# Optimization experiments

Hardware: AMD Instinct MI355X
Metric: run time of the kernel (lower is better)

The kernel has to match this reference:

```python
import jax, jax.numpy as jnp
import numpy as np

D_MODEL = 1024
N_HEADS = 16
HEAD_DIM = D_MODEL // N_HEADS
SOFTMAX_SCALE = 1.0 / np.sqrt(HEAD_DIM).astype(np.float32)


def setup_inputs() -> dict:
    key = jax.random.key(0)
    k1, k2, k3, k4, k5 = jax.random.split(key, 5)
    B, S = 2, 2048
    bound_qkv = 1.0 / np.sqrt(D_MODEL)
    x = jax.random.normal(k1, (B, S, D_MODEL), dtype=jnp.float32)
    # torch nn.Linear stores weight as [out_features, in_features]
    Wqkv_w = jax.random.uniform(k2, (3 * D_MODEL, D_MODEL), jnp.float32, -bound_qkv, bound_qkv)
    Wqkv_b = jax.random.uniform(k3, (3 * D_MODEL,), jnp.float32, -bound_qkv, bound_qkv)
    Wout_w = jax.random.uniform(k4, (D_MODEL, D_MODEL), jnp.float32, -bound_qkv, bound_qkv)
    Wout_b = jax.random.uniform(k5, (D_MODEL,), jnp.float32, -bound_qkv, bound_qkv)
    return {"x": x, "Wqkv_w": Wqkv_w, "Wqkv_b": Wqkv_b, "Wout_w": Wout_w, "Wout_b": Wout_b}


def reference(x, Wqkv_w, Wqkv_b, Wout_w, Wout_b):
    B, S, D = x.shape
    # fused QKV projection
    qkv = jnp.einsum('bsd,ed->bse', x, Wqkv_w) + Wqkv_b  # [B, S, 3D]
    q, k, v = jnp.split(qkv, 3, axis=2)
    # b s (h d) -> b h s d
    q = q.reshape(B, S, N_HEADS, HEAD_DIM).transpose(0, 2, 1, 3)
    k = k.reshape(B, S, N_HEADS, HEAD_DIM).transpose(0, 2, 1, 3)
    v = v.reshape(B, S, N_HEADS, HEAD_DIM).transpose(0, 2, 1, 3)
    attn = jnp.einsum('bhsd,bhtd->bhst', q, k) * SOFTMAX_SCALE
    attn = jax.nn.softmax(attn, axis=-1)
    ctx = jnp.einsum('bhst,bhtd->bhsd', attn, v)
    ctx = ctx.transpose(0, 2, 1, 3).reshape(B, S, D)
    out = jnp.einsum('bsd,ed->bse', ctx, Wout_w) + Wout_b
    return out
```

## Files before the change

kernel.cpp:

```cpp
#include <hip/hip_runtime.h>
#include <hip/hip_bf16.h>

typedef __attribute__((ext_vector_type(8))) __bf16 bfrag;
typedef __attribute__((ext_vector_type(4))) float f32x4;
typedef __attribute__((ext_vector_type(16))) float f32x16;
typedef __attribute__((ext_vector_type(8))) unsigned short u16x8;
typedef __attribute__((ext_vector_type(4))) unsigned short u16x4;
typedef __attribute__((ext_vector_type(4))) unsigned int u32x4;

#define SEQ 2048
#define NH 16
#define HD 64
#define DMODEL 1024
#define MTOT 4096
#define QSCALE 0.18033688011112042f

static __device__ __forceinline__ unsigned short f2bf(float f) {
  unsigned int u = __builtin_bit_cast(unsigned int, f);
  u += 0x7FFFu + ((u >> 16) & 1u);
  return (unsigned short)(u >> 16);
}

static __device__ __forceinline__ unsigned cvt_pk_bf16(float lo, float hi) {
  unsigned r;
  asm("v_cvt_pk_bf16_f32 %0, %1, %2" : "=v"(r) : "v"(lo), "v"(hi));
  return r;
}

static __device__ __forceinline__ float rmax16(const f32x16 v) {
  float a0 = fmaxf(v[0], v[1]), a1 = fmaxf(v[2], v[3]);
  float a2 = fmaxf(v[4], v[5]), a3 = fmaxf(v[6], v[7]);
  float a4 = fmaxf(v[8], v[9]), a5 = fmaxf(v[10], v[11]);
  float a6 = fmaxf(v[12], v[13]), a7 = fmaxf(v[14], v[15]);
  float b0 = fmaxf(a0, a1), b1 = fmaxf(a2, a3), b2 = fmaxf(a4, a5), b3 = fmaxf(a6, a7);
  return fmaxf(fmaxf(b0, b1), fmaxf(b2, b3));
}

static __device__ __forceinline__ float rsum16(const f32x16 v) {
  float a0 = v[0] + v[1], a1 = v[2] + v[3], a2 = v[4] + v[5], a3 = v[6] + v[7];
  float a4 = v[8] + v[9], a5 = v[10] + v[11], a6 = v[12] + v[13], a7 = v[14] + v[15];
  float b0 = a0 + a1, b1 = a2 + a3, b2 = a4 + a5, b3 = a6 + a7;
  return (b0 + b1) + (b2 + b3);
}

__global__ __launch_bounds__(256) void cvt_bf16_kernel(const float* __restrict__ in,
                                                       unsigned short* __restrict__ out,
                                                       int n8) {
  int i = blockIdx.x * 256 + threadIdx.x;
  if (i >= n8) return;
  const float4* p = reinterpret_cast<const float4*>(in) + (size_t)i * 2;
  float4 a = p[0], b = p[1];
  u16x8 o;
  o[0] = f2bf(a.x); o[1] = f2bf(a.y); o[2] = f2bf(a.z); o[3] = f2bf(a.w);
  o[4] = f2bf(b.x); o[5] = f2bf(b.y); o[6] = f2bf(b.z); o[7] = f2bf(b.w);
  *(reinterpret_cast<u16x8*>(out) + i) = o;
}

#define GLDS(gp, lp)                                                       \
  __builtin_amdgcn_global_load_lds(                                        \
      (const __attribute__((address_space(1))) void*)(gp),                 \
      (__attribute__((address_space(3))) void*)(lp), 16, 0, 0)

template <int EPI>
__global__ __launch_bounds__(256) void gemm_bt_kernel(
    const unsigned short* __restrict__ A, const unsigned short* __restrict__ B,
    const float* __restrict__ bias, unsigned short* __restrict__ q_out,
    unsigned short* __restrict__ k_out, unsigned short* __restrict__ v_out,
    float* __restrict__ f_out, int M, int N, int K) {
  __shared__ __align__(16) unsigned short As[128 * 32];
  __shared__ __align__(16) unsigned short Bs[128 * 32];
  const int t = threadIdx.x;
  const int l = t & 63, w = t >> 6;
  const int m0 = blockIdx.y * 128, n0 = blockIdx.x * 128;
  const int wrow = (w >> 1) * 64, wcol = (w & 1) * 64;
  const int lrow = l & 15, lk = (l >> 4) * 8;
  const int srow = t >> 2;
  const int scol = ((t & 3) ^ (srow & 3)) * 8;
  f32x4 acc[4][4] = {};
  for (int k0 = 0; k0 < K; k0 += 32) {
    __syncthreads();
    GLDS(A + (size_t)(m0 + srow) * K + k0 + scol, As + (size_t)t * 8);
    GLDS(A + (size_t)(m0 + srow + 64) * K + k0 + scol, As + 2048 + (size_t)t * 8);
    GLDS(B + (size_t)(n0 + srow) * K + k0 + scol, Bs + (size_t)t * 8);
    GLDS(B + (size_t)(n0 + srow + 64) * K + k0 + scol, Bs + 2048 + (size_t)t * 8);
    __syncthreads();
    bfrag af[4], bf[4];
#pragma unroll
    for (int mt = 0; mt < 4; ++mt) {
      int row = wrow + mt * 16 + lrow;
      af[mt] = *(const bfrag*)&As[row * 32 + (lk ^ ((row & 3) << 3))];
    }
#pragma unroll
    for (int nt = 0; nt < 4; ++nt) {
      int row = wcol + nt * 16 + lrow;
      bf[nt] = *(const bfrag*)&Bs[row * 32 + (lk ^ ((row & 3) << 3))];
    }
#pragma unroll
    for (int mt = 0; mt < 4; ++mt)
#pragma unroll
      for (int nt = 0; nt < 4; ++nt)
        acc[mt][nt] =
            __builtin_amdgcn_mfma_f32_16x16x32_bf16(af[mt], bf[nt], acc[mt][nt], 0, 0, 0);
  }
#pragma unroll
  for (int nt = 0; nt < 4; ++nt) {
    int gn = n0 + wcol + nt * 16 + lrow;
    float bv = bias[gn];
    if constexpr (EPI == 0) {
      int sel = gn >> 10;
      int e = gn & 1023;
      int h = e >> 6, d = e & 63;
#pragma unroll
      for (int mt = 0; mt < 4; ++mt) {
#pragma unroll
        for (int r = 0; r < 4; ++r) {
          int gm = m0 + wrow + mt * 16 + (l >> 4) * 4 + r;
          int b = gm >> 11, s = gm & 2047;
          float fv = acc[mt][nt][r] + bv;
          if (sel == 0)
            q_out[((size_t)(b * NH + h) * SEQ + s) * HD + d] = f2bf(fv * QSCALE);
          else if (sel == 1)
            k_out[((size_t)(b * NH + h) * SEQ + s) * HD + d] = f2bf(fv);
          else
            v_out[((size_t)(b * NH + h) * HD + d) * SEQ + s] = f2bf(fv);
        }
      }
    } else {
#pragma unroll
      for (int mt = 0; mt < 4; ++mt) {
#pragma unroll
        for (int r = 0; r < 4; ++r) {
          int gm = m0 + wrow + mt * 16 + (l >> 4) * 4 + r;
          f_out[(size_t)gm * N + gn] = acc[mt][nt][r] + bv;
        }
      }
    }
  }
}

__global__ __launch_bounds__(256, 2)
void attn_kernel(const unsigned short* __restrict__ Q,
                 const unsigned short* __restrict__ Km,
                 const unsigned short* __restrict__ Vt,
                 unsigned short* __restrict__ Ctx) {
  __shared__ __align__(16) unsigned short Ks[2][4096];
  __shared__ __align__(16) unsigned short Vs[2][4096];
  const int t = threadIdx.x;
  const int l = t & 63, w = t >> 6;
  const int q31 = l & 31, h = l >> 5;
  const int lid = blockIdx.y * gridDim.x + blockIdx.x;
  const int bh = (lid & 7) * 4 + ((lid >> 3) >> 4);
  const int q0 = ((lid >> 3) & 15) * 128 + w * 32;
  const unsigned short* qb = Q + (size_t)bh * SEQ * HD;
  const unsigned short* kb = Km + (size_t)bh * SEQ * HD;
  const unsigned short* vb = Vt + (size_t)bh * HD * SEQ;

  bfrag qf[4];
#pragma unroll
  for (int c = 0; c < 4; ++c)
    qf[c] = *(const bfrag*)&qb[(size_t)(q0 + q31) * HD + c * 16 + h * 8];

  f32x16 acc0 = {}, acc1 = {};
  float m = -3e38f, lsum = 0.f;

  const int srow = t >> 3;
  const int ssw = ((t & 7) ^ (srow & 7)) * 8;

  GLDS(kb + (size_t)srow * HD + ssw, &Ks[0][0] + t * 8);
  GLDS(kb + (size_t)(32 + srow) * HD + ssw, &Ks[0][0] + 2048 + t * 8);
  GLDS(vb + (size_t)srow * SEQ + ssw, &Vs[0][0] + t * 8);
  GLDS(vb + (size_t)(32 + srow) * SEQ + ssw, &Vs[0][0] + 2048 + t * 8);
  __syncthreads();

  const int swz = q31 & 7;

#pragma unroll 1
  for (int t2 = 0; t2 < 32; ++t2) {
    const unsigned short* Kc = &Ks[t2 & 1][0];
    const unsigned short* Vc = &Vs[t2 & 1][0];
    if (t2 < 31) {
      unsigned short* kd = &Ks[(t2 + 1) & 1][0];
      unsigned short* vd = &Vs[(t2 + 1) & 1][0];
      const int kvn = (t2 + 1) * 64;
      GLDS(kb + (size_t)(kvn + srow) * HD + ssw, kd + t * 8);
      GLDS(kb + (size_t)(kvn + 32 + srow) * HD + ssw, kd + 2048 + t * 8);
      GLDS(vb + (size_t)srow * SEQ + kvn + ssw, vd + t * 8);
      GLDS(vb + (size_t)(32 + srow) * SEQ + kvn + ssw, vd + 2048 + t * 8);
    }
    bfrag kf[8], vf[8];
#pragma unroll
    for (int i = 0; i < 8; ++i) {
      const int off = ((i >> 2) * 32 + q31) * 64 + ((((i & 3) * 2 + h) ^ swz) * 8);
      kf[i] = *(const bfrag*)&Kc[off];
      vf[i] = *(const bfrag*)&Vc[off];
    }
    f32x16 s0 = {}, s1 = {};
#pragma unroll
    for (int c = 0; c < 4; ++c) {
      s0 = __builtin_amdgcn_mfma_f32_32x32x16_bf16(kf[c], qf[c], s0, 0, 0, 0);
      s1 = __builtin_amdgcn_mfma_f32_32x32x16_bf16(kf[4 + c], qf[c], s1, 0, 0, 0);
    }
    float tm = fmaxf(rmax16(s0), rmax16(s1));
    tm = fmaxf(tm, __shfl_xor(tm, 32));
    if (!__all(tm - m <= 8.f)) {
      float mn = fmaxf(m, tm);
      float al = __builtin_amdgcn_exp2f(m - mn);
      m = mn;
      lsum *= al;
#pragma unroll
      for (int r = 0; r < 16; ++r) {
        acc0[r] *= al;
        acc1[r] *= al;
      }
    }
#pragma unroll
    for (int r = 0; r < 16; ++r) s0[r] = __builtin_amdgcn_exp2f(s0[r] - m);
#pragma unroll
    for (int r = 0; r < 16; ++r) s1[r] = __builtin_amdgcn_exp2f(s1[r] - m);
    float ps = rsum16(s0) + rsum16(s1);
    ps += __shfl_xor(ps, 32);
    lsum += ps;
#pragma unroll
    for (int cg = 0; cg < 4; ++cg) {
      const f32x16 sv = (cg < 2) ? s0 : s1;
      const int bse = (cg & 1) * 8;
      unsigned pk0 = cvt_pk_bf16(sv[bse + 0], sv[bse + 1]);
      unsigned pk1 = cvt_pk_bf16(sv[bse + 2], sv[bse + 3]);
      unsigned pk2 = cvt_pk_bf16(sv[bse + 4], sv[bse + 5]);
      unsigned pk3 = cvt_pk_bf16(sv[bse + 6], sv[bse + 7]);
      auto w02 = __builtin_amdgcn_permlane32_swap(pk0, pk2, false, false);
      auto w13 = __builtin_amdgcn_permlane32_swap(pk1, pk3, false, false);
      u32x4 bw = {(unsigned)w02[0], (unsigned)w13[0], (unsigned)w02[1], (unsigned)w13[1]};
      bfrag pb = __builtin_bit_cast(bfrag, bw);
      acc0 = __builtin_amdgcn_mfma_f32_32x32x16_bf16(vf[cg], pb, acc0, 0, 0, 0);
      acc1 = __builtin_amdgcn_mfma_f32_32x32x16_bf16(vf[4 + cg], pb, acc1, 0, 0, 0);
    }
    __syncthreads();
  }

  const int b = bh >> 4, head = bh & 15;
  const float inv = __builtin_amdgcn_rcpf(lsum);
  unsigned short* cp = Ctx + ((size_t)(b * SEQ + (q0 + q31)) * NH + head) * HD;
#pragma unroll
  for (int dt = 0; dt < 2; ++dt) {
    const f32x16 av = dt ? acc1 : acc0;
#pragma unroll
    for (int rq = 0; rq < 4; ++rq) {
      u16x4 o;
#pragma unroll
      for (int rr = 0; rr < 4; ++rr) o[rr] = f2bf(av[rq * 4 + rr] * inv);
      *(u16x4*)&cp[dt * 32 + rq * 8 + h * 4] = o;
    }
  }
}

extern "C" void kernel_launch(void* const* d_in, const int* in_sizes, int n_in,
                              void* d_out, int out_size, void* d_ws, size_t ws_size,
                              hipStream_t stream) {
  const float* x = (const float*)d_in[0];
  const float* wqkv = (const float*)d_in[1];
  const float* bqkv = (const float*)d_in[2];
  const float* wout = (const float*)d_in[3];
  const float* bout = (const float*)d_in[4];
  float* out = (float*)d_out;

  unsigned short* xb = (unsigned short*)d_ws;
  unsigned short* wqkvb = xb + (size_t)MTOT * DMODEL;
  unsigned short* woutb = wqkvb + (size_t)3 * DMODEL * DMODEL;
  unsigned short* qb = woutb + (size_t)DMODEL * DMODEL;
  unsigned short* kb = qb + (size_t)32 * SEQ * HD;
  unsigned short* vtb = kb + (size_t)32 * SEQ * HD;
  unsigned short* ctxb = vtb + (size_t)32 * SEQ * HD;

  {
    int n8 = MTOT * DMODEL / 8;
    cvt_bf16_kernel<<<(n8 + 255) / 256, 256, 0, stream>>>(x, xb, n8);
  }
  {
    int n8 = 3 * DMODEL * DMODEL / 8;
    cvt_bf16_kernel<<<(n8 + 255) / 256, 256, 0, stream>>>(wqkv, wqkvb, n8);
  }
  {
    int n8 = DMODEL * DMODEL / 8;
    cvt_bf16_kernel<<<(n8 + 255) / 256, 256, 0, stream>>>(wout, woutb, n8);
  }
  gemm_bt_kernel<0><<<dim3(3 * DMODEL / 128, MTOT / 128), 256, 0, stream>>>(
      xb, wqkvb, bqkv, qb, kb, vtb, nullptr, MTOT, 3 * DMODEL, DMODEL);
  attn_kernel<<<dim3(SEQ / 128, 32), 256, 0, stream>>>(qb, kb, vtb, ctxb);
  gemm_bt_kernel<1><<<dim3(DMODEL / 128, MTOT / 128), 256, 0, stream>>>(
      ctxb, woutb, bout, nullptr, nullptr, nullptr, out, MTOT, DMODEL, DMODEL);
}
```

Baseline: 137.7 us.

## Triple-buffer LDS staging in GEMM and attention with vmcnt-based waits

```diff
diff --git a/kernel.cpp b/kernel.cpp
--- a/kernel.cpp
+++ b/kernel.cpp
@@ -67,8 +67,8 @@
     const float* __restrict__ bias, unsigned short* __restrict__ q_out,
     unsigned short* __restrict__ k_out, unsigned short* __restrict__ v_out,
     float* __restrict__ f_out, int M, int N, int K) {
-  __shared__ __align__(16) unsigned short As[128 * 32];
-  __shared__ __align__(16) unsigned short Bs[128 * 32];
+  __shared__ __align__(16) unsigned short As[3][4096];
+  __shared__ __align__(16) unsigned short Bs[3][4096];
   const int t = threadIdx.x;
   const int l = t & 63, w = t >> 6;
   const int m0 = blockIdx.y * 128, n0 = blockIdx.x * 128;
@@ -77,23 +77,41 @@
   const int srow = t >> 2;
   const int scol = ((t & 3) ^ (srow & 3)) * 8;
   f32x4 acc[4][4] = {};
-  for (int k0 = 0; k0 < K; k0 += 32) {
-    __syncthreads();
-    GLDS(A + (size_t)(m0 + srow) * K + k0 + scol, As + (size_t)t * 8);
-    GLDS(A + (size_t)(m0 + srow + 64) * K + k0 + scol, As + 2048 + (size_t)t * 8);
-    GLDS(B + (size_t)(n0 + srow) * K + k0 + scol, Bs + (size_t)t * 8);
-    GLDS(B + (size_t)(n0 + srow + 64) * K + k0 + scol, Bs + 2048 + (size_t)t * 8);
-    __syncthreads();
+
+#define GSTAGE(buf, K0)                                                     \
+  do {                                                                      \
+    GLDS(A + (size_t)(m0 + srow) * K + (K0) + scol, &As[buf][0] + t * 8);   \
+    GLDS(A + (size_t)(m0 + srow + 64) * K + (K0) + scol,                    \
+         &As[buf][0] + 2048 + t * 8);                                       \
+    GLDS(B + (size_t)(n0 + srow) * K + (K0) + scol, &Bs[buf][0] + t * 8);   \
+    GLDS(B + (size_t)(n0 + srow + 64) * K + (K0) + scol,                    \
+         &Bs[buf][0] + 2048 + t * 8);                                       \
+  } while (0)
+
+  const int nsteps = K >> 5;
+  GSTAGE(0, 0);
+  GSTAGE(1, 32);
+#pragma unroll 1
+  for (int ks = 0; ks < nsteps; ++ks) {
+    if (ks < nsteps - 1)
+      asm volatile("s_waitcnt vmcnt(4)" ::: "memory");
+    else
+      asm volatile("s_waitcnt vmcnt(0)" ::: "memory");
+    __builtin_amdgcn_s_barrier();
+    __builtin_amdgcn_sched_barrier(0);
+    if (ks + 2 < nsteps) GSTAGE((ks + 2) % 3, (ks + 2) * 32);
+    const unsigned short* Ac = &As[ks % 3][0];
+    const unsigned short* Bc = &Bs[ks % 3][0];
     bfrag af[4], bf[4];
 #pragma unroll
     for (int mt = 0; mt < 4; ++mt) {
       int row = wrow + mt * 16 + lrow;
-      af[mt] = *(const bfrag*)&As[row * 32 + (lk ^ ((row & 3) << 3))];
+      af[mt] = *(const bfrag*)&Ac[row * 32 + (lk ^ ((row & 3) << 3))];
     }
 #pragma unroll
     for (int nt = 0; nt < 4; ++nt) {
       int row = wcol + nt * 16 + lrow;
-      bf[nt] = *(const bfrag*)&Bs[row * 32 + (lk ^ ((row & 3) << 3))];
+      bf[nt] = *(const bfrag*)&Bc[row * 32 + (lk ^ ((row & 3) << 3))];
     }
 #pragma unroll
     for (int mt = 0; mt < 4; ++mt)
@@ -102,6 +120,7 @@
         acc[mt][nt] =
             __builtin_amdgcn_mfma_f32_16x16x32_bf16(af[mt], bf[nt], acc[mt][nt], 0, 0, 0);
   }
+#undef GSTAGE
 #pragma unroll
   for (int nt = 0; nt < 4; ++nt) {
     int gn = n0 + wcol + nt * 16 + lrow;
@@ -143,8 +162,8 @@
                  const unsigned short* __restrict__ Km,
                  const unsigned short* __restrict__ Vt,
                  unsigned short* __restrict__ Ctx) {
-  __shared__ __align__(16) unsigned short Ks[2][4096];
-  __shared__ __align__(16) unsigned short Vs[2][4096];
+  __shared__ __align__(16) unsigned short Ks[3][4096];
+  __shared__ __align__(16) unsigned short Vs[3][4096];
   const int t = threadIdx.x;
   const int l = t & 63, w = t >> 6;
   const int q31 = l & 31, h = l >> 5;
@@ -166,27 +185,33 @@
   const int srow = t >> 3;
   const int ssw = ((t & 7) ^ (srow & 7)) * 8;
 
-  GLDS(kb + (size_t)srow * HD + ssw, &Ks[0][0] + t * 8);
-  GLDS(kb + (size_t)(32 + srow) * HD + ssw, &Ks[0][0] + 2048 + t * 8);
-  GLDS(vb + (size_t)srow * SEQ + ssw, &Vs[0][0] + t * 8);
-  GLDS(vb + (size_t)(32 + srow) * SEQ + ssw, &Vs[0][0] + 2048 + t * 8);
-  __syncthreads();
+#define STAGE(buf, T)                                                        \
+  do {                                                                       \
+    const int kv0_ = (T) * 64;                                               \
+    GLDS(kb + (size_t)(kv0_ + srow) * HD + ssw, &Ks[buf][0] + t * 8);        \
+    GLDS(kb + (size_t)(kv0_ + 32 + srow) * HD + ssw,                         \
+         &Ks[buf][0] + 2048 + t * 8);                                        \
+    GLDS(vb + (size_t)srow * SEQ + kv0_ + ssw, &Vs[buf][0] + t * 8);         \
+    GLDS(vb + (size_t)(32 + srow) * SEQ + kv0_ + ssw,                        \
+         &Vs[buf][0] + 2048 + t * 8);                                        \
+  } while (0)
+
+  STAGE(0, 0);
+  STAGE(1, 1);
 
   const int swz = q31 & 7;
 
 #pragma unroll 1
   for (int t2 = 0; t2 < 32; ++t2) {
-    const unsigned short* Kc = &Ks[t2 & 1][0];
-    const unsigned short* Vc = &Vs[t2 & 1][0];
-    if (t2 < 31) {
-      unsigned short* kd = &Ks[(t2 + 1) & 1][0];
-      unsigned short* vd = &Vs[(t2 + 1) & 1][0];
-      const int kvn = (t2 + 1) * 64;
-      GLDS(kb + (size_t)(kvn + srow) * HD + ssw, kd + t * 8);
-      GLDS(kb + (size_t)(kvn + 32 + srow) * HD + ssw, kd + 2048 + t * 8);
-      GLDS(vb + (size_t)srow * SEQ + kvn + ssw, vd + t * 8);
-      GLDS(vb + (size_t)(32 + srow) * SEQ + kvn + ssw, vd + 2048 + t * 8);
-    }
+    if (t2 < 31)
+      asm volatile("s_waitcnt vmcnt(4)" ::: "memory");
+    else
+      asm volatile("s_waitcnt vmcnt(0)" ::: "memory");
+    __builtin_amdgcn_s_barrier();
+    __builtin_amdgcn_sched_barrier(0);
+    if (t2 < 30) STAGE((t2 + 2) % 3, t2 + 2);
+    const unsigned short* Kc = &Ks[t2 % 3][0];
+    const unsigned short* Vc = &Vs[t2 % 3][0];
     bfrag kf[8], vf[8];
 #pragma unroll
     for (int i = 0; i < 8; ++i) {
@@ -195,11 +220,13 @@
       vf[i] = *(const bfrag*)&Vc[off];
     }
     f32x16 s0 = {}, s1 = {};
+    __builtin_amdgcn_s_setprio(1);
 #pragma unroll
     for (int c = 0; c < 4; ++c) {
       s0 = __builtin_amdgcn_mfma_f32_32x32x16_bf16(kf[c], qf[c], s0, 0, 0, 0);
       s1 = __builtin_amdgcn_mfma_f32_32x32x16_bf16(kf[4 + c], qf[c], s1, 0, 0, 0);
     }
+    __builtin_amdgcn_s_setprio(0);
     float tm = fmaxf(rmax16(s0), rmax16(s1));
     tm = fmaxf(tm, __shfl_xor(tm, 32));
     if (!__all(tm - m <= 8.f)) {
@@ -220,6 +247,7 @@
     float ps = rsum16(s0) + rsum16(s1);
     ps += __shfl_xor(ps, 32);
     lsum += ps;
+    __builtin_amdgcn_s_setprio(1);
 #pragma unroll
     for (int cg = 0; cg < 4; ++cg) {
       const f32x16 sv = (cg < 2) ? s0 : s1;
@@ -235,8 +263,9 @@
       acc0 = __builtin_amdgcn_mfma_f32_32x32x16_bf16(vf[cg], pb, acc0, 0, 0, 0);
       acc1 = __builtin_amdgcn_mfma_f32_32x32x16_bf16(vf[4 + cg], pb, acc1, 0, 0, 0);
     }
-    __syncthreads();
-  }
+    __builtin_amdgcn_s_setprio(0);
+  }
+#undef STAGE
 
   const int b = bh >> 4, head = bh & 15;
   const float inv = __builtin_amdgcn_rcpf(lsum);
```

Result: no change. 136.2 us (-1.1%).
